# Performance work log

Measured on AMD Instinct MI355X. Metric: run time of the kernel, lower is better.

Reference implementation:

```python
import jax, jax.numpy as jnp
import numpy as np

B, N, D = 2, 2048, 512
H, HD = 8, 64
R = 64  # graph_radius
SCALE = HD ** -0.5
LN_EPS = 1e-5


def _ln(x, g, b):
    m = jnp.mean(x, axis=-1, keepdims=True)
    v = jnp.mean((x - m) ** 2, axis=-1, keepdims=True)
    return (x - m) * jax.lax.rsqrt(v + LN_EPS) * g + b


def setup_inputs() -> dict:
    key = jax.random.key(0)
    ks = jax.random.split(key, 8)
    w = lambda k, shape: (jax.random.normal(k, shape, jnp.float32) * 0.02)
    return {
        "nodes": jax.random.normal(ks[0], (B, N, D), jnp.float32),
        "ln1_g": jnp.ones((D,), jnp.float32), "ln1_b": jnp.zeros((D,), jnp.float32),
        "qkv_w": w(ks[1], (D, 3 * D)), "qkv_b": jnp.zeros((3 * D,), jnp.float32),
        "proj_w": w(ks[2], (D, D)), "proj_b": jnp.zeros((D,), jnp.float32),
        "rep_scale": jnp.ones((H,), jnp.float32),
        "rel_bias": w(ks[3], (2 * N - 1, H)),
        "ln2_g": jnp.ones((D,), jnp.float32), "ln2_b": jnp.zeros((D,), jnp.float32),
        "mlp_w1": w(ks[4], (D, 2 * D)), "mlp_b1": jnp.zeros((2 * D,), jnp.float32),
        "mlp_w2": w(ks[5], (2 * D, D)), "mlp_b2": jnp.zeros((D,), jnp.float32),
    }


def reference(nodes, ln1_g, ln1_b, qkv_w, qkv_b, proj_w, proj_b, rep_scale,
              rel_bias, ln2_g, ln2_b, mlp_w1, mlp_b1, mlp_w2, mlp_b2):
    b, n, d = nodes.shape
    x = _ln(nodes, ln1_g, ln1_b)                       # [B,N,D]
    qkv = (x @ qkv_w + qkv_b).reshape(b, n, 3, H, HD)
    qkv = jnp.transpose(qkv, (2, 0, 3, 1, 4))          # [3,B,H,N,HD]
    q, k, v = qkv[0], qkv[1], qkv[2]
    logits = jnp.einsum('bhnd,bhmd->bhnm', q, k) * SCALE
    # representation correlation (F.normalize with eps=1e-12)
    rep = x / jnp.maximum(jnp.linalg.norm(x, axis=-1, keepdims=True), 1e-12)
    corr = jnp.einsum('bnd,bmd->bnm', rep, rep)        # [B,N,N]
    logits = logits + corr[:, None] * rep_scale[None, :, None, None]
    pos = jnp.arange(n)
    relidx = pos[:, None] - pos[None, :]               # [N,N]
    bias = rel_bias[relidx + n - 1]                    # [N,N,H]
    logits = logits + jnp.transpose(bias, (2, 0, 1))[None]
    mask = jnp.abs(relidx) <= R
    logits = jnp.where(mask[None, None], logits, -jnp.inf)
    attn = jax.nn.softmax(logits, axis=-1)
    upd = jnp.einsum('bhnm,bhmd->bnhd', attn, v).reshape(b, n, d)
    nodes = nodes + (upd @ proj_w + proj_b)
    y = _ln(nodes, ln2_g, ln2_b)
    h = jax.nn.gelu(y @ mlp_w1 + mlp_b1, approximate=False)
    return nodes + (h @ mlp_w2 + mlp_b2)
```

## Files before the change

kernel.cpp:

```cpp
#include <hip/hip_runtime.h>
#include <math.h>

typedef __bf16 bf16;
typedef __bf16 bf16x4 __attribute__((ext_vector_type(4)));
typedef __bf16 bf16x8 __attribute__((ext_vector_type(8)));
typedef float floatx4 __attribute__((ext_vector_type(4)));

#define BB 2
#define NN 2048
#define DD 512
#define HH 8
#define HD 64
#define RR 64
#define D3 1536
#define NEG_BIG (-1e30f)
#define TQ 32
#define TBAND 160

#define GL2LDS16(g, l)                                                        \
    __builtin_amdgcn_global_load_lds(                                         \
        (const __attribute__((address_space(1))) void*)(const void*)(g),      \
        (__attribute__((address_space(3))) void*)(void*)(l), 16, 0, 0)

__global__ __launch_bounds__(256) void cvt_all_kernel(
    const float* __restrict__ qkv_w, const float* __restrict__ proj_w,
    const float* __restrict__ m1w, const float* __restrict__ m2w,
    bf16* __restrict__ wqt, bf16* __restrict__ wpt,
    bf16* __restrict__ w1t, bf16* __restrict__ w2t) {
    __shared__ bf16 Ts[64][72];
    const int tid = threadIdx.x;
    int bid = blockIdx.x;
    const float* W; bf16* Wt; int K, N, bx, by;
    if (bid < 192)      { W = qkv_w;  Wt = wqt; K = 512;  N = 1536; bx = bid % 24; by = bid / 24; }
    else if (bid < 256) { bid -= 192; W = proj_w; Wt = wpt; K = 512;  N = 512;  bx = bid % 8;  by = bid / 8; }
    else if (bid < 384) { bid -= 256; W = m1w;  Wt = w1t; K = 512;  N = 1024; bx = bid % 16; by = bid / 16; }
    else                { bid -= 384; W = m2w;  Wt = w2t; K = 1024; N = 512;  bx = bid % 8;  by = bid / 8; }
    const int n0 = bx * 64, k0 = by * 64;
    #pragma unroll
    for (int i = 0; i < 4; i++) {
        int r = (tid >> 4) + i * 16;
        int c = (tid & 15) * 4;
        floatx4 v = *(const floatx4*)(W + (size_t)(k0 + r) * N + n0 + c);
        #pragma unroll
        for (int e = 0; e < 4; e++) Ts[r][c + e] = (bf16)v[e];
    }
    __syncthreads();
    #pragma unroll
    for (int i = 0; i < 4; i++) {
        int n = (tid >> 4) + i * 16;
        int k = (tid & 15) * 4;
        bf16x4 o;
        #pragma unroll
        for (int e = 0; e < 4; e++) o[e] = Ts[k + e][n];
        *(bf16x4*)(Wt + (size_t)(n0 + n) * K + k0 + k) = o;
    }
}

__device__ inline float block_reduce_sum256(float v, float* sbuf) {
    const int tid = threadIdx.x;
    #pragma unroll
    for (int o = 32; o > 0; o >>= 1) v += __shfl_xor(v, o, 64);
    __syncthreads();
    if ((tid & 63) == 0) sbuf[tid >> 6] = v;
    __syncthreads();
    return sbuf[0] + sbuf[1] + sbuf[2] + sbuf[3];
}

template <bool WANT_INV>
__global__ __launch_bounds__(256) void ln_kernel(
    const float* __restrict__ in, const float* __restrict__ gw,
    const float* __restrict__ bw, bf16* __restrict__ out,
    float* __restrict__ invnorm) {
    __shared__ float sbuf[4];
    const int row = blockIdx.x, tid = threadIdx.x;
    const int i0 = tid * 2;
    const float* ip = in + (size_t)row * DD;
    float v0 = ip[i0], v1 = ip[i0 + 1];
    float mean = block_reduce_sum256(v0 + v1, sbuf) * (1.f / DD);
    float d0 = v0 - mean, d1 = v1 - mean;
    float var = block_reduce_sum256(d0 * d0 + d1 * d1, sbuf) * (1.f / DD);
    float rs = rsqrtf(var + 1e-5f);
    float x0 = d0 * rs * gw[i0] + bw[i0];
    float x1 = d1 * rs * gw[i0 + 1] + bw[i0 + 1];
    out[(size_t)row * DD + i0] = (bf16)x0;
    out[(size_t)row * DD + i0 + 1] = (bf16)x1;
    if (WANT_INV) {
        float s2 = block_reduce_sum256(x0 * x0 + x1 * x1, sbuf);
        if (tid == 0) invnorm[row] = 1.f / fmaxf(sqrtf(s2), 1e-12f);
    }
}

template <int MODE>
__global__ __launch_bounds__(256) void gemm_bt(
    const bf16* __restrict__ A, const bf16* __restrict__ Bt,
    const float* __restrict__ bias, const float* __restrict__ resid,
    void* __restrict__ out, int M, int N, int K) {
    __shared__ __align__(16) bf16 As[2][64 * 64];
    __shared__ __align__(16) bf16 Bs[2][64 * 64];
    const int tid = threadIdx.x;
    const int w = tid >> 6, lane = tid & 63;
    const int lr = lane & 15, lq = lane >> 4;
    const int rowBase = blockIdx.y * 64, colBase = blockIdx.x * 64;
    const int wm = (w >> 1) * 32, wn = (w & 1) * 32;

    floatx4 acc[2][2];
    #pragma unroll
    for (int i = 0; i < 2; i++)
        #pragma unroll
        for (int j = 0; j < 2; j++) acc[i][j] = (floatx4){0.f, 0.f, 0.f, 0.f};

    auto stage = [&](int buf, int k0) {
        #pragma unroll
        for (int i = 0; i < 2; i++) {
            int g = i * 256 + tid;
            int row = g >> 3, k8 = (g & 7) ^ (row & 7);
            GL2LDS16(A + (size_t)(rowBase + row) * K + k0 + k8 * 8, &As[buf][g * 8]);
        }
        #pragma unroll
        for (int i = 0; i < 2; i++) {
            int g = i * 256 + tid;
            int row = g >> 3, k8 = (g & 7) ^ (row & 7);
            GL2LDS16(Bt + (size_t)(colBase + row) * K + k0 + k8 * 8, &Bs[buf][g * 8]);
        }
    };

    const int nsteps = K >> 6;
    stage(0, 0);
    for (int s = 0; s < nsteps; s++) {
        __syncthreads();
        if (s + 1 < nsteps) stage((s + 1) & 1, (s + 1) * 64);
        const int buf = s & 1;
        #pragma unroll
        for (int kb = 0; kb < 2; kb++) {
            bf16x8 af[2], bfr[2];
            #pragma unroll
            for (int i = 0; i < 2; i++) {
                int row = wm + i * 16 + lr;
                int g = row * 8 + ((kb * 4 + lq) ^ (row & 7));
                af[i] = *(bf16x8*)&As[buf][g * 8];
            }
            #pragma unroll
            for (int j = 0; j < 2; j++) {
                int row = wn + j * 16 + lr;
                int g = row * 8 + ((kb * 4 + lq) ^ (row & 7));
                bfr[j] = *(bf16x8*)&Bs[buf][g * 8];
            }
            #pragma unroll
            for (int i = 0; i < 2; i++)
                #pragma unroll
                for (int j = 0; j < 2; j++)
                    acc[i][j] = __builtin_amdgcn_mfma_f32_16x16x32_bf16(
                        af[i], bfr[j], acc[i][j], 0, 0, 0);
        }
    }

    #pragma unroll
    for (int i = 0; i < 2; i++) {
        #pragma unroll
        for (int j = 0; j < 2; j++) {
            #pragma unroll
            for (int r = 0; r < 4; r++) {
                int row = rowBase + wm + i * 16 + lq * 4 + r;
                int col = colBase + wn + j * 16 + lr;
                size_t idx = (size_t)row * N + col;
                float v = acc[i][j][r] + bias[col];
                if (MODE == 0) {
                    ((bf16*)out)[idx] = (bf16)v;
                } else if (MODE == 1) {
                    ((float*)out)[idx] = v + resid[idx];
                } else if (MODE == 2) {
                    float g = 0.5f * v * (1.f + erff(v * 0.70710678118654752f));
                    ((bf16*)out)[idx] = (bf16)g;
                } else {
                    ((float*)out)[idx] = v + resid[idx];
                }
            }
        }
    }
}

__global__ __launch_bounds__(256) void corr_kernel(
    const bf16* __restrict__ x, const float* __restrict__ invnorm,
    float* __restrict__ corr_g) {
    __shared__ __align__(16) bf16 Xc[TBAND * 72];
    __shared__ float invb[TBAND];
    const int tid = threadIdx.x;
    const int b = blockIdx.x & 1, n0 = (blockIdx.x >> 1) * TQ;
    const int bN = b * NN;
    const int w = tid >> 6, lane = tid & 63;
    const int lr = lane & 15, lq = lane >> 4;
    const int rowHalf = (w >> 1) * 16, colBase = (w & 1) * 80;

    if (tid < TBAND) {
        int mc = min(max(n0 - RR + tid, 0), NN - 1);
        invb[tid] = invnorm[bN + mc];
    }

    floatx4 cacc[5];
    #pragma unroll
    for (int t = 0; t < 5; t++) cacc[t] = (floatx4){0.f, 0.f, 0.f, 0.f};

    for (int c = 0; c < 8; c++) {
        __syncthreads();
        #pragma unroll
        for (int rr = 0; rr < 6; rr++) {
            int G = rr * 256 + tid;
            if (G < 1440) {
                int j = G / 9, gc = G % 9;
                int gcs = min(gc, 7);
                int mc = min(max(n0 - RR + j, 0), NN - 1);
                GL2LDS16(x + (size_t)(bN + mc) * DD + c * 64 + gcs * 8, Xc + G * 8);
            }
        }
        __syncthreads();
        #pragma unroll
        for (int kb = 0; kb < 2; kb++) {
            bf16x8 a = *(bf16x8*)&Xc[(64 + rowHalf + lr) * 72 + kb * 32 + lq * 8];
            #pragma unroll
            for (int t = 0; t < 5; t++) {
                bf16x8 bb = *(bf16x8*)&Xc[(colBase + t * 16 + lr) * 72 + kb * 32 + lq * 8];
                cacc[t] = __builtin_amdgcn_mfma_f32_16x16x32_bf16(a, bb, cacc[t], 0, 0, 0);
            }
        }
    }

    float invq[4];
    #pragma unroll
    for (int r = 0; r < 4; r++) invq[r] = invb[64 + rowHalf + lq * 4 + r];
    const size_t cbase = (size_t)blockIdx.x * TQ * TBAND;
    #pragma unroll
    for (int t = 0; t < 5; t++) {
        float invk = invb[colBase + t * 16 + lr];
        #pragma unroll
        for (int r = 0; r < 4; r++)
            corr_g[cbase + (size_t)(rowHalf + lq * 4 + r) * TBAND + colBase + t * 16 + lr] =
                cacc[t][r] * invq[r] * invk;
    }
}

__global__ __launch_bounds__(256) void vtrans_kernel(
    const bf16* __restrict__ qkvb, bf16* __restrict__ vt_g) {
    __shared__ bf16 Ts[64][72];
    const int tid = threadIdx.x;
    const int r0 = blockIdx.x * 64;
    const int h = blockIdx.y;
    #pragma unroll
    for (int i = 0; i < 2; i++) {
        int r = (tid >> 3) + i * 32, c8 = tid & 7;
        *(bf16x8*)&Ts[r][c8 * 8] =
            *(const bf16x8*)(qkvb + (size_t)(r0 + r) * D3 + 2 * DD + h * HD + c8 * 8);
    }
    __syncthreads();
    #pragma unroll
    for (int i = 0; i < 2; i++) {
        int d = (tid >> 3) + i * 32, c8 = (tid & 7) * 8;
        bf16x8 o;
        #pragma unroll
        for (int e = 0; e < 8; e++) o[e] = Ts[c8 + e][d];
        *(bf16x8*)(vt_g + (((size_t)(h * HD + d)) << 12) + r0 + c8) = o;
    }
}

__global__ __launch_bounds__(256) void attn_kernel(
    const bf16* __restrict__ qkv, const bf16* __restrict__ vt_g,
    const float* __restrict__ corr_g, const float* __restrict__ rep_scale,
    const float* __restrict__ rel_bias, bf16* __restrict__ upd) {
    __shared__ __align__(16) bf16 Qs[TQ * 264];
    __shared__ __align__(16) bf16 Ks[TBAND * 72];
    __shared__ __align__(16) bf16 Vt[64 * 168];
    __shared__ __align__(16) bf16 Ps[TQ * 168];
    __shared__ float relb[4][192];
    __shared__ float rmax2[TQ][2];
    __shared__ float rsum2[TQ][2];

    const int tid = threadIdx.x;
    const int bid = blockIdx.x;
    const int b = bid & 1;
    const int h0 = ((bid >> 1) & 1) * 4;
    const int n0 = (bid >> 2) * TQ;
    const int bN = b * NN;
    const int w = tid >> 6, lane = tid & 63;
    const int lr = lane & 15, lq = lane >> 4;
    const int rowHalf = (w >> 1) * 16;
    const int colBase = (w & 1) * 80;
    const int c2 = (w & 1) * 32;

    for (int idx = tid; idx < 4 * 191; idx += 256) {
        int hh = idx / 191, dh = idx - hh * 191;
        relb[hh][dh] = rel_bias[(size_t)(dh + (NN - 1 - 95)) * HH + h0 + hh];
    }

    float corrv[5][4];
    {
        const size_t cbase = (size_t)(((bid >> 2) << 1) | b) * TQ * TBAND;
        #pragma unroll
        for (int t = 0; t < 5; t++)
            #pragma unroll
            for (int r = 0; r < 4; r++)
                corrv[t][r] = corr_g[cbase + (size_t)(rowHalf + lq * 4 + r) * TBAND +
                                     colBase + t * 16 + lr];
    }

    #pragma unroll
    for (int rr = 0; rr < 5; rr++) {
        int G = rr * 256 + tid;
        if (G < 1056) {
            int q = G / 33, gc = G % 33;
            int gcs = min(gc, 31);
            GL2LDS16(qkv + (size_t)(bN + n0 + q) * D3 + h0 * HD + gcs * 8, Qs + G * 8);
        }
    }

    for (int h = h0; h < h0 + 4; h++) {
        __syncthreads();
        #pragma unroll
        for (int rr = 0; rr < 6; rr++) {
            int G = rr * 256 + tid;
            if (G < 1440) {
                int j = G / 9, gc = G % 9;
                int gcs = min(gc, 7);
                int mc = min(max(n0 - RR + j, 0), NN - 1);
                GL2LDS16(qkv + (size_t)(bN + mc) * D3 + DD + h * HD + gcs * 8, Ks + G * 8);
            }
        }
        #pragma unroll
        for (int rr = 0; rr < 6; rr++) {
            int G = rr * 256 + tid;
            if (G < 1344) {
                int d = G / 21, gc = G % 21;
                int nsrc = min(max(n0 - RR + gc * 8, 0), NN - 8);
                GL2LDS16(vt_g + (((size_t)(h * HD + d)) << 12) + bN + nsrc, Vt + G * 8);
            }
        }
        __syncthreads();

        floatx4 sacc[5];
        #pragma unroll
        for (int t = 0; t < 5; t++) sacc[t] = (floatx4){0.f, 0.f, 0.f, 0.f};
        #pragma unroll
        for (int kb = 0; kb < 2; kb++) {
            bf16x8 a = *(bf16x8*)&Qs[(rowHalf + lr) * 264 + (h - h0) * 64 + kb * 32 + lq * 8];
            #pragma unroll
            for (int t = 0; t < 5; t++) {
                bf16x8 bb = *(bf16x8*)&Ks[(colBase + t * 16 + lr) * 72 + kb * 32 + lq * 8];
                sacc[t] = __builtin_amdgcn_mfma_f32_16x16x32_bf16(a, bb, sacc[t], 0, 0, 0);
            }
        }

        const float srep = rep_scale[h];
        float l[5][4];
        float mx[4] = {NEG_BIG, NEG_BIG, NEG_BIG, NEG_BIG};
        #pragma unroll
        for (int t = 0; t < 5; t++) {
            int j = colBase + t * 16 + lr;
            int m = n0 - RR + j;
            #pragma unroll
            for (int r = 0; r < 4; r++) {
                int qi = rowHalf + lq * 4 + r;
                int relidx = qi + RR - j;
                bool valid = (relidx >= -RR) && (relidx <= RR) && (m >= 0) && (m < NN);
                float lv = sacc[t][r] * 0.125f + corrv[t][r] * srep +
                           relb[h - h0][relidx + 95];
                l[t][r] = valid ? lv : NEG_BIG;
                mx[r] = fmaxf(mx[r], l[t][r]);
            }
        }
        #pragma unroll
        for (int r = 0; r < 4; r++)
            #pragma unroll
            for (int mk = 1; mk <= 8; mk <<= 1)
                mx[r] = fmaxf(mx[r], __shfl_xor(mx[r], mk, 64));
        if (lr == 0) {
            #pragma unroll
            for (int r = 0; r < 4; r++) rmax2[rowHalf + lq * 4 + r][w & 1] = mx[r];
        }
        __syncthreads();

        float rm[4], sm[4];
        #pragma unroll
        for (int r = 0; r < 4; r++) {
            int row = rowHalf + lq * 4 + r;
            rm[r] = fmaxf(rmax2[row][0], rmax2[row][1]);
            sm[r] = 0.f;
        }
        #pragma unroll
        for (int t = 0; t < 5; t++) {
            int j = colBase + t * 16 + lr;
            #pragma unroll
            for (int r = 0; r < 4; r++) {
                float pv = __expf(l[t][r] - rm[r]);
                sm[r] += pv;
                Ps[(rowHalf + lq * 4 + r) * 168 + j] = (bf16)pv;
            }
        }
        #pragma unroll
        for (int r = 0; r < 4; r++)
            #pragma unroll
            for (int mk = 1; mk <= 8; mk <<= 1)
                sm[r] += __shfl_xor(sm[r], mk, 64);
        if (lr == 0) {
            #pragma unroll
            for (int r = 0; r < 4; r++) rsum2[rowHalf + lq * 4 + r][w & 1] = sm[r];
        }
        __syncthreads();

        floatx4 oacc[2] = {(floatx4){0.f, 0.f, 0.f, 0.f}, (floatx4){0.f, 0.f, 0.f, 0.f}};
        #pragma unroll
        for (int kb = 0; kb < 5; kb++) {
            bf16x8 a = *(bf16x8*)&Ps[(rowHalf + lr) * 168 + kb * 32 + lq * 8];
            #pragma unroll
            for (int tt = 0; tt < 2; tt++) {
                bf16x8 bb = *(bf16x8*)&Vt[(c2 + tt * 16 + lr) * 168 + kb * 32 + lq * 8];
                oacc[tt] = __builtin_amdgcn_mfma_f32_16x16x32_bf16(a, bb, oacc[tt], 0, 0, 0);
            }
        }
        #pragma unroll
        for (int r = 0; r < 4; r++) {
            int row = rowHalf + lq * 4 + r;
            float rinv = 1.f / (rsum2[row][0] + rsum2[row][1]);
            #pragma unroll
            for (int tt = 0; tt < 2; tt++) {
                upd[(size_t)(bN + n0 + row) * DD + h * HD + c2 + tt * 16 + lr] =
                    (bf16)(oacc[tt][r] * rinv);
            }
        }
    }
}

extern "C" void kernel_launch(void* const* d_in, const int* in_sizes, int n_in,
                              void* d_out, int out_size, void* d_ws,
                              size_t ws_size, hipStream_t stream) {
    const float* nodes  = (const float*)d_in[0];
    const float* ln1_g  = (const float*)d_in[1];
    const float* ln1_b  = (const float*)d_in[2];
    const float* qkv_w  = (const float*)d_in[3];
    const float* qkv_b  = (const float*)d_in[4];
    const float* proj_w = (const float*)d_in[5];
    const float* proj_b = (const float*)d_in[6];
    const float* rep_s  = (const float*)d_in[7];
    const float* rel_b  = (const float*)d_in[8];
    const float* ln2_g  = (const float*)d_in[9];
    const float* ln2_b  = (const float*)d_in[10];
    const float* mlp_w1 = (const float*)d_in[11];
    const float* mlp_b1 = (const float*)d_in[12];
    const float* mlp_w2 = (const float*)d_in[13];
    const float* mlp_b2 = (const float*)d_in[14];

    char* p = (char*)d_ws;
    float* invn = (float*)p;            p += (size_t)1 << 20;
    bf16*  wqt  = (bf16*)p;             p += (size_t)DD * D3 * 2;
    bf16*  wpt  = (bf16*)p;             p += (size_t)DD * DD * 2;
    bf16*  w1t  = (bf16*)p;             p += (size_t)DD * 2 * DD * 2;
    bf16*  w2t  = (bf16*)p;             p += (size_t)2 * DD * DD * 2;
    bf16*  x    = (bf16*)p;             p += (size_t)BB * NN * DD * 2;
    bf16*  qkvb = (bf16*)p;             p += (size_t)BB * NN * D3 * 2;
    char*  regA = p;                    p += (size_t)BB * NN * DD * 4;
    float* corr_g = (float*)regA;
    bf16*  vt_g   = (bf16*)(regA + (size_t)BB * (NN / TQ) * TQ * TBAND * 4);
    float* mid    = (float*)regA;
    bf16*  y    = x;
    bf16*  hgl  = qkvb;
    bf16*  upd  = (bf16*)d_out;

    const int M = BB * NN;

    cvt_all_kernel<<<512, 256, 0, stream>>>(qkv_w, proj_w, mlp_w1, mlp_w2,
                                            wqt, wpt, w1t, w2t);
    ln_kernel<true><<<M, 256, 0, stream>>>(nodes, ln1_g, ln1_b, x, invn);
    corr_kernel<<<BB * (NN / TQ), 256, 0, stream>>>(x, invn, corr_g);
    gemm_bt<0><<<dim3(D3 / 64, M / 64), 256, 0, stream>>>(
        x, wqt, qkv_b, nullptr, qkvb, M, D3, DD);
    vtrans_kernel<<<dim3(M / 64, HH), 256, 0, stream>>>(qkvb, vt_g);
    attn_kernel<<<(NN / TQ) * 2 * BB, 256, 0, stream>>>(
        qkvb, vt_g, corr_g, rep_s, rel_b, upd);
    gemm_bt<1><<<dim3(DD / 64, M / 64), 256, 0, stream>>>(
        upd, wpt, proj_b, nodes, mid, M, DD, DD);
    ln_kernel<false><<<M, 256, 0, stream>>>(mid, ln2_g, ln2_b, y, nullptr);
    gemm_bt<2><<<dim3(2 * DD / 64, M / 64), 256, 0, stream>>>(
        y, w1t, mlp_b1, nullptr, hgl, M, 2 * DD, DD);
    gemm_bt<3><<<dim3(DD / 64, M / 64), 256, 0, stream>>>(
        hgl, w2t, mlp_b2, mid, (float*)d_out, M, DD, 2 * DD);
}
```

Before: 179.2 us.

## Merge weight conversion with LN1, fuse QKV GEMM with corr and V transpose

The weight-conversion kernel and the first layernorm now run as one launch, with extra blocks each handling 8 LN rows. The QKV GEMM, the correlation band kernel and the V transpose are merged into one launch: GEMM blocks for the V columns transpose through shared memory and write V-transposed directly, which removes the separate vtrans pass and its re-read of qkvb. The attention grid is split to 2 heads per block instead of 4, doubling the block count to 512 for more parallelism at the cost of reloading K/V bands and corr more often. The intent is fewer launches and better GPU fill, with the risk of uneven block workloads inside the merged kernels.

```diff
diff --git a/kernel.cpp b/kernel.cpp
--- a/kernel.cpp
+++ b/kernel.cpp
@@ -22,41 +22,7 @@
         (const __attribute__((address_space(1))) void*)(const void*)(g),      \
         (__attribute__((address_space(3))) void*)(void*)(l), 16, 0, 0)
 
-__global__ __launch_bounds__(256) void cvt_all_kernel(
-    const float* __restrict__ qkv_w, const float* __restrict__ proj_w,
-    const float* __restrict__ m1w, const float* __restrict__ m2w,
-    bf16* __restrict__ wqt, bf16* __restrict__ wpt,
-    bf16* __restrict__ w1t, bf16* __restrict__ w2t) {
-    __shared__ bf16 Ts[64][72];
-    const int tid = threadIdx.x;
-    int bid = blockIdx.x;
-    const float* W; bf16* Wt; int K, N, bx, by;
-    if (bid < 192)      { W = qkv_w;  Wt = wqt; K = 512;  N = 1536; bx = bid % 24; by = bid / 24; }
-    else if (bid < 256) { bid -= 192; W = proj_w; Wt = wpt; K = 512;  N = 512;  bx = bid % 8;  by = bid / 8; }
-    else if (bid < 384) { bid -= 256; W = m1w;  Wt = w1t; K = 512;  N = 1024; bx = bid % 16; by = bid / 16; }
-    else                { bid -= 384; W = m2w;  Wt = w2t; K = 1024; N = 512;  bx = bid % 8;  by = bid / 8; }
-    const int n0 = bx * 64, k0 = by * 64;
-    #pragma unroll
-    for (int i = 0; i < 4; i++) {
-        int r = (tid >> 4) + i * 16;
-        int c = (tid & 15) * 4;
-        floatx4 v = *(const floatx4*)(W + (size_t)(k0 + r) * N + n0 + c);
-        #pragma unroll
-        for (int e = 0; e < 4; e++) Ts[r][c + e] = (bf16)v[e];
-    }
-    __syncthreads();
-    #pragma unroll
-    for (int i = 0; i < 4; i++) {
-        int n = (tid >> 4) + i * 16;
-        int k = (tid & 15) * 4;
-        bf16x4 o;
-        #pragma unroll
-        for (int e = 0; e < 4; e++) o[e] = Ts[k + e][n];
-        *(bf16x4*)(Wt + (size_t)(n0 + n) * K + k0 + k) = o;
-    }
-}
-
-__device__ inline float block_reduce_sum256(float v, float* sbuf) {
+static __device__ __forceinline__ float block_reduce_sum256(float v, float* sbuf) {
     const int tid = threadIdx.x;
     #pragma unroll
     for (int o = 32; o > 0; o >>= 1) v += __shfl_xor(v, o, 64);
@@ -66,13 +32,10 @@
     return sbuf[0] + sbuf[1] + sbuf[2] + sbuf[3];
 }
 
-template <bool WANT_INV>
-__global__ __launch_bounds__(256) void ln_kernel(
-    const float* __restrict__ in, const float* __restrict__ gw,
-    const float* __restrict__ bw, bf16* __restrict__ out,
-    float* __restrict__ invnorm) {
-    __shared__ float sbuf[4];
-    const int row = blockIdx.x, tid = threadIdx.x;
+static __device__ __forceinline__ void ln_row(
+    float* sbuf, const float* in, const float* gw, const float* bw,
+    bf16* out, float* invnorm, int row, bool want_inv) {
+    const int tid = threadIdx.x;
     const int i0 = tid * 2;
     const float* ip = in + (size_t)row * DD;
     float v0 = ip[i0], v1 = ip[i0 + 1];
@@ -84,9 +47,213 @@
     float x1 = d1 * rs * gw[i0 + 1] + bw[i0 + 1];
     out[(size_t)row * DD + i0] = (bf16)x0;
     out[(size_t)row * DD + i0 + 1] = (bf16)x1;
-    if (WANT_INV) {
+    if (want_inv) {
         float s2 = block_reduce_sum256(x0 * x0 + x1 * x1, sbuf);
         if (tid == 0) invnorm[row] = 1.f / fmaxf(sqrtf(s2), 1e-12f);
+    }
+}
+
+union SMemCL {
+    bf16 Ts[64][72];
+    float sbuf[4];
+};
+__global__ __launch_bounds__(256) void cvt_ln_kernel(
+    const float* __restrict__ qkv_w, const float* __restrict__ proj_w,
+    const float* __restrict__ m1w, const float* __restrict__ m2w,
+    bf16* __restrict__ wqt, bf16* __restrict__ wpt,
+    bf16* __restrict__ w1t, bf16* __restrict__ w2t,
+    const float* __restrict__ nodes, const float* __restrict__ ln1_g,
+    const float* __restrict__ ln1_b, bf16* __restrict__ x,
+    float* __restrict__ invn) {
+    __shared__ SMemCL sm;
+    const int tid = threadIdx.x;
+    int bid = blockIdx.x;
+    if (bid >= 512) {
+        int r0 = (bid - 512) * 8;
+        for (int r = 0; r < 8; r++)
+            ln_row(sm.sbuf, nodes, ln1_g, ln1_b, x, invn, r0 + r, true);
+        return;
+    }
+    const float* W; bf16* Wt; int K, N, bx, by;
+    if (bid < 192)      { W = qkv_w; Wt = wqt; K = 512;  N = 1536; bx = bid % 24; by = bid / 24; }
+    else if (bid < 256) { bid -= 192; W = proj_w; Wt = wpt; K = 512;  N = 512;  bx = bid % 8;  by = bid / 8; }
+    else if (bid < 384) { bid -= 256; W = m1w; Wt = w1t; K = 512;  N = 1024; bx = bid % 16; by = bid / 16; }
+    else                { bid -= 384; W = m2w; Wt = w2t; K = 1024; N = 512;  bx = bid % 8;  by = bid / 8; }
+    const int n0 = bx * 64, k0 = by * 64;
+    #pragma unroll
+    for (int i = 0; i < 4; i++) {
+        int r = (tid >> 4) + i * 16;
+        int c = (tid & 15) * 4;
+        floatx4 v = *(const floatx4*)(W + (size_t)(k0 + r) * N + n0 + c);
+        #pragma unroll
+        for (int e = 0; e < 4; e++) sm.Ts[r][c + e] = (bf16)v[e];
+    }
+    __syncthreads();
+    #pragma unroll
+    for (int i = 0; i < 4; i++) {
+        int n = (tid >> 4) + i * 16;
+        int k = (tid & 15) * 4;
+        bf16x4 o;
+        #pragma unroll
+        for (int e = 0; e < 4; e++) o[e] = sm.Ts[k + e][n];
+        *(bf16x4*)(Wt + (size_t)(n0 + n) * K + k0 + k) = o;
+    }
+}
+
+union SMemQC {
+    struct { bf16 As[2][4096], Bs[2][4096]; } g;
+    struct { bf16 Ts[64][72]; } t;
+    struct { bf16 Xc[TBAND * 72]; float invb[TBAND]; } c;
+};
+__global__ __launch_bounds__(256) void qkv_corr_kernel(
+    const bf16* __restrict__ x, const bf16* __restrict__ wqt,
+    const float* __restrict__ qkv_b, const float* __restrict__ invn,
+    bf16* __restrict__ qkvb, bf16* __restrict__ vt_g,
+    float* __restrict__ corr_g) {
+    __shared__ SMemQC sm;
+    const int tid = threadIdx.x;
+    const int bid = blockIdx.x;
+    const int w = tid >> 6, lane = tid & 63;
+    const int lr = lane & 15, lq = lane >> 4;
+
+    if (bid >= 1536) {
+        const int item = bid - 1536;
+        const int b = item & 1, n0 = (item >> 1) * TQ;
+        const int bN = b * NN;
+        const int rowHalf = (w >> 1) * 16, colBase = (w & 1) * 80;
+        if (tid < TBAND) {
+            int mc = min(max(n0 - RR + tid, 0), NN - 1);
+            sm.c.invb[tid] = invn[bN + mc];
+        }
+        floatx4 cacc[5];
+        #pragma unroll
+        for (int t = 0; t < 5; t++) cacc[t] = (floatx4){0.f, 0.f, 0.f, 0.f};
+        for (int c = 0; c < 8; c++) {
+            __syncthreads();
+            #pragma unroll
+            for (int rr = 0; rr < 6; rr++) {
+                int G = rr * 256 + tid;
+                if (G < 1440) {
+                    int j = G / 9, gc = G % 9;
+                    int gcs = min(gc, 7);
+                    int mc = min(max(n0 - RR + j, 0), NN - 1);
+                    GL2LDS16(x + (size_t)(bN + mc) * DD + c * 64 + gcs * 8, sm.c.Xc + G * 8);
+                }
+            }
+            __syncthreads();
+            #pragma unroll
+            for (int kb = 0; kb < 2; kb++) {
+                bf16x8 a = *(bf16x8*)&sm.c.Xc[(64 + rowHalf + lr) * 72 + kb * 32 + lq * 8];
+                #pragma unroll
+                for (int t = 0; t < 5; t++) {
+                    bf16x8 bb = *(bf16x8*)&sm.c.Xc[(colBase + t * 16 + lr) * 72 + kb * 32 + lq * 8];
+                    cacc[t] = __builtin_amdgcn_mfma_f32_16x16x32_bf16(a, bb, cacc[t], 0, 0, 0);
+                }
+            }
+        }
+        float invq[4];
+        #pragma unroll
+        for (int r = 0; r < 4; r++) invq[r] = sm.c.invb[64 + rowHalf + lq * 4 + r];
+        const size_t cbase = (size_t)item * TQ * TBAND;
+        #pragma unroll
+        for (int t = 0; t < 5; t++) {
+            float invk = sm.c.invb[colBase + t * 16 + lr];
+            #pragma unroll
+            for (int r = 0; r < 4; r++)
+                corr_g[cbase + (size_t)(rowHalf + lq * 4 + r) * TBAND + colBase + t * 16 + lr] =
+                    cacc[t][r] * invq[r] * invk;
+        }
+        return;
+    }
+
+    const int bx = bid % 24, by = bid / 24;
+    const int rowBase = by * 64, colBase = bx * 64;
+    const int wm = (w >> 1) * 32, wn = (w & 1) * 32;
+
+    floatx4 acc[2][2];
+    #pragma unroll
+    for (int i = 0; i < 2; i++)
+        #pragma unroll
+        for (int j = 0; j < 2; j++) acc[i][j] = (floatx4){0.f, 0.f, 0.f, 0.f};
+
+    auto stage = [&](int buf, int k0) {
+        #pragma unroll
+        for (int i = 0; i < 2; i++) {
+            int g = i * 256 + tid;
+            int row = g >> 3, k8 = (g & 7) ^ (row & 7);
+            GL2LDS16(x + (size_t)(rowBase + row) * DD + k0 + k8 * 8, &sm.g.As[buf][g * 8]);
+        }
+        #pragma unroll
+        for (int i = 0; i < 2; i++) {
+            int g = i * 256 + tid;
+            int row = g >> 3, k8 = (g & 7) ^ (row & 7);
+            GL2LDS16(wqt + (size_t)(colBase + row) * DD + k0 + k8 * 8, &sm.g.Bs[buf][g * 8]);
+        }
+    };
+
+    stage(0, 0);
+    for (int s = 0; s < 8; s++) {
+        __syncthreads();
+        if (s + 1 < 8) stage((s + 1) & 1, (s + 1) * 64);
+        const int buf = s & 1;
+        #pragma unroll
+        for (int kb = 0; kb < 2; kb++) {
+            bf16x8 af[2], bfr[2];
+            #pragma unroll
+            for (int i = 0; i < 2; i++) {
+                int row = wm + i * 16 + lr;
+                int g = row * 8 + ((kb * 4 + lq) ^ (row & 7));
+                af[i] = *(bf16x8*)&sm.g.As[buf][g * 8];
+            }
+            #pragma unroll
+            for (int j = 0; j < 2; j++) {
+                int row = wn + j * 16 + lr;
+                int g = row * 8 + ((kb * 4 + lq) ^ (row & 7));
+                bfr[j] = *(bf16x8*)&sm.g.Bs[buf][g * 8];
+            }
+            #pragma unroll
+            for (int i = 0; i < 2; i++)
+                #pragma unroll
+                for (int j = 0; j < 2; j++)
+                    acc[i][j] = __builtin_amdgcn_mfma_f32_16x16x32_bf16(
+                        af[i], bfr[j], acc[i][j], 0, 0, 0);
+        }
+    }
+
+    if (bx < 16) {
+        #pragma unroll
+        for (int i = 0; i < 2; i++)
+            #pragma unroll
+            for (int j = 0; j < 2; j++)
+                #pragma unroll
+                for (int r = 0; r < 4; r++) {
+                    int row = rowBase + wm + i * 16 + lq * 4 + r;
+                    int col = colBase + wn + j * 16 + lr;
+                    qkvb[(size_t)row * D3 + col] = (bf16)(acc[i][j][r] + qkv_b[col]);
+                }
+    } else {
+        __syncthreads();
+        #pragma unroll
+        for (int i = 0; i < 2; i++)
+            #pragma unroll
+            for (int j = 0; j < 2; j++)
+                #pragma unroll
+                for (int r = 0; r < 4; r++) {
+                    int nl = wm + i * 16 + lq * 4 + r;
+                    int dl = wn + j * 16 + lr;
+                    sm.t.Ts[nl][dl] = (bf16)(acc[i][j][r] + qkv_b[colBase + dl]);
+                }
+        __syncthreads();
+        const int dV = colBase - 1024;
+        #pragma unroll
+        for (int i2 = 0; i2 < 2; i2++) {
+            int d = (tid >> 3) + i2 * 32;
+            int n8 = (tid & 7) * 8;
+            bf16x8 o;
+            #pragma unroll
+            for (int e = 0; e < 8; e++) o[e] = sm.t.Ts[n8 + e][d];
+            *(bf16x8*)(vt_g + (((size_t)(dV + d)) << 12) + rowBase + n8) = o;
+        }
     }
 }
 
@@ -164,9 +331,7 @@
                 int col = colBase + wn + j * 16 + lr;
                 size_t idx = (size_t)row * N + col;
                 float v = acc[i][j][r] + bias[col];
-                if (MODE == 0) {
-                    ((bf16*)out)[idx] = (bf16)v;
-                } else if (MODE == 1) {
+                if (MODE == 1) {
                     ((float*)out)[idx] = v + resid[idx];
                 } else if (MODE == 2) {
                     float g = 0.5f * v * (1.f + erff(v * 0.70710678118654752f));
@@ -179,105 +344,30 @@
     }
 }
 
-__global__ __launch_bounds__(256) void corr_kernel(
-    const bf16* __restrict__ x, const float* __restrict__ invnorm,
-    float* __restrict__ corr_g) {
-    __shared__ __align__(16) bf16 Xc[TBAND * 72];
-    __shared__ float invb[TBAND];
-    const int tid = threadIdx.x;
-    const int b = blockIdx.x & 1, n0 = (blockIdx.x >> 1) * TQ;
-    const int bN = b * NN;
-    const int w = tid >> 6, lane = tid & 63;
-    const int lr = lane & 15, lq = lane >> 4;
-    const int rowHalf = (w >> 1) * 16, colBase = (w & 1) * 80;
-
-    if (tid < TBAND) {
-        int mc = min(max(n0 - RR + tid, 0), NN - 1);
-        invb[tid] = invnorm[bN + mc];
-    }
-
-    floatx4 cacc[5];
-    #pragma unroll
-    for (int t = 0; t < 5; t++) cacc[t] = (floatx4){0.f, 0.f, 0.f, 0.f};
-
-    for (int c = 0; c < 8; c++) {
-        __syncthreads();
-        #pragma unroll
-        for (int rr = 0; rr < 6; rr++) {
-            int G = rr * 256 + tid;
-            if (G < 1440) {
-                int j = G / 9, gc = G % 9;
-                int gcs = min(gc, 7);
-                int mc = min(max(n0 - RR + j, 0), NN - 1);
-                GL2LDS16(x + (size_t)(bN + mc) * DD + c * 64 + gcs * 8, Xc + G * 8);
-            }
-        }
-        __syncthreads();
-        #pragma unroll
-        for (int kb = 0; kb < 2; kb++) {
-            bf16x8 a = *(bf16x8*)&Xc[(64 + rowHalf + lr) * 72 + kb * 32 + lq * 8];
-            #pragma unroll
-            for (int t = 0; t < 5; t++) {
-                bf16x8 bb = *(bf16x8*)&Xc[(colBase + t * 16 + lr) * 72 + kb * 32 + lq * 8];
-                cacc[t] = __builtin_amdgcn_mfma_f32_16x16x32_bf16(a, bb, cacc[t], 0, 0, 0);
-            }
-        }
-    }
-
-    float invq[4];
-    #pragma unroll
-    for (int r = 0; r < 4; r++) invq[r] = invb[64 + rowHalf + lq * 4 + r];
-    const size_t cbase = (size_t)blockIdx.x * TQ * TBAND;
-    #pragma unroll
-    for (int t = 0; t < 5; t++) {
-        float invk = invb[colBase + t * 16 + lr];
-        #pragma unroll
-        for (int r = 0; r < 4; r++)
-            corr_g[cbase + (size_t)(rowHalf + lq * 4 + r) * TBAND + colBase + t * 16 + lr] =
-                cacc[t][r] * invq[r] * invk;
-    }
-}
-
-__global__ __launch_bounds__(256) void vtrans_kernel(
-    const bf16* __restrict__ qkvb, bf16* __restrict__ vt_g) {
-    __shared__ bf16 Ts[64][72];
-    const int tid = threadIdx.x;
-    const int r0 = blockIdx.x * 64;
-    const int h = blockIdx.y;
-    #pragma unroll
-    for (int i = 0; i < 2; i++) {
-        int r = (tid >> 3) + i * 32, c8 = tid & 7;
-        *(bf16x8*)&Ts[r][c8 * 8] =
-            *(const bf16x8*)(qkvb + (size_t)(r0 + r) * D3 + 2 * DD + h * HD + c8 * 8);
-    }
-    __syncthreads();
-    #pragma unroll
-    for (int i = 0; i < 2; i++) {
-        int d = (tid >> 3) + i * 32, c8 = (tid & 7) * 8;
-        bf16x8 o;
-        #pragma unroll
-        for (int e = 0; e < 8; e++) o[e] = Ts[c8 + e][d];
-        *(bf16x8*)(vt_g + (((size_t)(h * HD + d)) << 12) + r0 + c8) = o;
-    }
+__global__ __launch_bounds__(256) void ln2_kernel(
+    const float* __restrict__ in, const float* __restrict__ gw,
+    const float* __restrict__ bw, bf16* __restrict__ out) {
+    __shared__ float sbuf[4];
+    ln_row(sbuf, in, gw, bw, out, nullptr, blockIdx.x, false);
 }
 
 __global__ __launch_bounds__(256) void attn_kernel(
     const bf16* __restrict__ qkv, const bf16* __restrict__ vt_g,
     const float* __restrict__ corr_g, const float* __restrict__ rep_scale,
     const float* __restrict__ rel_bias, bf16* __restrict__ upd) {
-    __shared__ __align__(16) bf16 Qs[TQ * 264];
+    __shared__ __align__(16) bf16 Qs[TQ * 136];
     __shared__ __align__(16) bf16 Ks[TBAND * 72];
     __shared__ __align__(16) bf16 Vt[64 * 168];
     __shared__ __align__(16) bf16 Ps[TQ * 168];
-    __shared__ float relb[4][192];
+    __shared__ float relb[2][192];
     __shared__ float rmax2[TQ][2];
     __shared__ float rsum2[TQ][2];
 
     const int tid = threadIdx.x;
-    const int bid = blockIdx.x;
-    const int b = bid & 1;
-    const int h0 = ((bid >> 1) & 1) * 4;
-    const int n0 = (bid >> 2) * TQ;
+    const int item = blockIdx.x;
+    const int b = item & 1;
+    const int h0 = ((item >> 1) & 3) * 2;
+    const int n0 = (item >> 3) * TQ;
     const int bN = b * NN;
     const int w = tid >> 6, lane = tid & 63;
     const int lr = lane & 15, lq = lane >> 4;
@@ -285,14 +375,14 @@
     const int colBase = (w & 1) * 80;
     const int c2 = (w & 1) * 32;
 
-    for (int idx = tid; idx < 4 * 191; idx += 256) {
+    for (int idx = tid; idx < 2 * 191; idx += 256) {
         int hh = idx / 191, dh = idx - hh * 191;
         relb[hh][dh] = rel_bias[(size_t)(dh + (NN - 1 - 95)) * HH + h0 + hh];
     }
 
     float corrv[5][4];
     {
-        const size_t cbase = (size_t)(((bid >> 2) << 1) | b) * TQ * TBAND;
+        const size_t cbase = (size_t)((((item >> 3)) << 1) | b) * TQ * TBAND;
         #pragma unroll
         for (int t = 0; t < 5; t++)
             #pragma unroll
@@ -302,16 +392,16 @@
     }
 
     #pragma unroll
-    for (int rr = 0; rr < 5; rr++) {
+    for (int rr = 0; rr < 3; rr++) {
         int G = rr * 256 + tid;
-        if (G < 1056) {
-            int q = G / 33, gc = G % 33;
-            int gcs = min(gc, 31);
+        if (G < 544) {
+            int q = G / 17, gc = G % 17;
+            int gcs = min(gc, 15);
             GL2LDS16(qkv + (size_t)(bN + n0 + q) * D3 + h0 * HD + gcs * 8, Qs + G * 8);
         }
     }
 
-    for (int h = h0; h < h0 + 4; h++) {
+    for (int h = h0; h < h0 + 2; h++) {
         __syncthreads();
         #pragma unroll
         for (int rr = 0; rr < 6; rr++) {
@@ -339,7 +429,7 @@
         for (int t = 0; t < 5; t++) sacc[t] = (floatx4){0.f, 0.f, 0.f, 0.f};
         #pragma unroll
         for (int kb = 0; kb < 2; kb++) {
-            bf16x8 a = *(bf16x8*)&Qs[(rowHalf + lr) * 264 + (h - h0) * 64 + kb * 32 + lq * 8];
+            bf16x8 a = *(bf16x8*)&Qs[(rowHalf + lr) * 136 + (h - h0) * 64 + kb * 32 + lq * 8];
             #pragma unroll
             for (int t = 0; t < 5; t++) {
                 bf16x8 bb = *(bf16x8*)&Ks[(colBase + t * 16 + lr) * 72 + kb * 32 + lq * 8];
@@ -376,12 +466,12 @@
         }
         __syncthreads();
 
-        float rm[4], sm[4];
+        float rm[4], sme[4];
         #pragma unroll
         for (int r = 0; r < 4; r++) {
             int row = rowHalf + lq * 4 + r;
             rm[r] = fmaxf(rmax2[row][0], rmax2[row][1]);
-            sm[r] = 0.f;
+            sme[r] = 0.f;
         }
         #pragma unroll
         for (int t = 0; t < 5; t++) {
@@ -389,7 +479,7 @@
             #pragma unroll
             for (int r = 0; r < 4; r++) {
                 float pv = __expf(l[t][r] - rm[r]);
-                sm[r] += pv;
+                sme[r] += pv;
                 Ps[(rowHalf + lq * 4 + r) * 168 + j] = (bf16)pv;
             }
         }
@@ -397,10 +487,10 @@
         for (int r = 0; r < 4; r++)
             #pragma unroll
             for (int mk = 1; mk <= 8; mk <<= 1)
-                sm[r] += __shfl_xor(sm[r], mk, 64);
+                sme[r] += __shfl_xor(sme[r], mk, 64);
         if (lr == 0) {
             #pragma unroll
-            for (int r = 0; r < 4; r++) rsum2[rowHalf + lq * 4 + r][w & 1] = sm[r];
+            for (int r = 0; r < 4; r++) rsum2[rowHalf + lq * 4 + r][w & 1] = sme[r];
         }
         __syncthreads();
 
@@ -464,18 +554,16 @@
 
     const int M = BB * NN;
 
-    cvt_all_kernel<<<512, 256, 0, stream>>>(qkv_w, proj_w, mlp_w1, mlp_w2,
-                                            wqt, wpt, w1t, w2t);
-    ln_kernel<true><<<M, 256, 0, stream>>>(nodes, ln1_g, ln1_b, x, invn);
-    corr_kernel<<<BB * (NN / TQ), 256, 0, stream>>>(x, invn, corr_g);
-    gemm_bt<0><<<dim3(D3 / 64, M / 64), 256, 0, stream>>>(
-        x, wqt, qkv_b, nullptr, qkvb, M, D3, DD);
-    vtrans_kernel<<<dim3(M / 64, HH), 256, 0, stream>>>(qkvb, vt_g);
-    attn_kernel<<<(NN / TQ) * 2 * BB, 256, 0, stream>>>(
+    cvt_ln_kernel<<<1024, 256, 0, stream>>>(
+        qkv_w, proj_w, mlp_w1, mlp_w2, wqt, wpt, w1t, w2t,
+        nodes, ln1_g, ln1_b, x, invn);
+    qkv_corr_kernel<<<1664, 256, 0, stream>>>(
+        x, wqt, qkv_b, invn, qkvb, vt_g, corr_g);
+    attn_kernel<<<512, 256, 0, stream>>>(
         qkvb, vt_g, corr_g, rep_s, rel_b, upd);
     gemm_bt<1><<<dim3(DD / 64, M / 64), 256, 0, stream>>>(
         upd, wpt, proj_b, nodes, mid, M, DD, DD);
-    ln_kernel<false><<<M, 256, 0, stream>>>(mid, ln2_g, ln2_b, y, nullptr);
+    ln2_kernel<<<M, 256, 0, stream>>>(mid, ln2_g, ln2_b, y);
     gemm_bt<2><<<dim3(2 * DD / 64, M / 64), 256, 0, stream>>>(
         y, w1t, mlp_b1, nullptr, hgl, M, 2 * DD, DD);
     gemm_bt<3><<<dim3(DD / 64, M / 64), 256, 0, stream>>>(
```

Measured after the change: 185.7 us. 1.04x slower.
